# Kernel optimization log

Hardware: AMD Instinct MI355X
Metric: run time of the kernel (lower is better)

Reference implementation:

```python
import jax, jax.numpy as jnp
import numpy as np

B, S, D = 4, 4096, 256


def setup_inputs() -> dict:
    key = jax.random.key(0)
    k1, k2, k3 = jax.random.split(key, 3)
    x = jax.random.normal(k1, (B, S, D), dtype=jnp.float32)
    w_int = jax.random.randint(k2, (D, D), 0, 127, dtype=jnp.int32)  # quantized weight (out, in)
    scale = jax.random.uniform(k3, (D,), dtype=jnp.float32)          # per-output-channel scale
    return {"x": x, "w_int": w_int, "scale": scale}


def reference(x, w_int, scale):
    # self-attention: q = k = v = x, single head over feature dim D
    inv_sqrt_d = 1.0 / jnp.sqrt(jnp.asarray(D, dtype=x.dtype))
    scores = jnp.einsum('bqd,bkd->bqk', x, x) * inv_sqrt_d   # [B,S,S]
    probs = jax.nn.softmax(scores, axis=-1)
    attn = jnp.einsum('bqk,bkd->bqd', probs, x)              # [B,S,D]
    # quantized linear: dequantize then matmul (y = attn @ W^T)
    W = w_int.astype(x.dtype) * scale[:, None]               # [D_out, D_in]
    return jnp.einsum('bsd,od->bso', attn, W)
```

## Files before the change

kernel.cpp:

```cpp
#include <hip/hip_runtime.h>

typedef __bf16 bf16x8 __attribute__((ext_vector_type(8)));
typedef float f32x16 __attribute__((ext_vector_type(16)));
typedef unsigned short u16x8 __attribute__((ext_vector_type(8)));

constexpr int B = 4, S = 4096, D = 256;
constexpr float CSC = 0.09016844005556021f;

static __device__ __forceinline__ unsigned short f2bf(float f) {
  unsigned int u = __builtin_bit_cast(unsigned int, f);
  u = (u + 0x7fffu + ((u >> 16) & 1u)) >> 16;
  return (unsigned short)u;
}

static __device__ __forceinline__ float bf2f(unsigned short u) {
  unsigned int v = ((unsigned int)u) << 16;
  return __builtin_bit_cast(float, v);
}

static __device__ __forceinline__ unsigned int pk2bf(float lo, float hi) {
  unsigned int r;
  asm("v_cvt_pk_bf16_f32 %0, %1, %2" : "=v"(r) : "v"(lo), "v"(hi));
  return r;
}

static __device__ __forceinline__ void gld16(const void* g, void* l) {
  __builtin_amdgcn_global_load_lds(
      (const __attribute__((address_space(1))) unsigned int*)g,
      (__attribute__((address_space(3))) unsigned int*)l, 16, 0, 0);
}

#define FENCE_ALL()                                               \
  do {                                                            \
    asm volatile("s_waitcnt vmcnt(0) lgkmcnt(0)" ::: "memory");   \
    __builtin_amdgcn_s_barrier();                                 \
    asm volatile("" ::: "memory");                                \
  } while (0)

__global__ __launch_bounds__(256) void k_prep(const float* __restrict__ x,
                                              unsigned short* __restrict__ xbf,
                                              unsigned short* __restrict__ xK,
                                              unsigned short* __restrict__ xV) {
  __shared__ unsigned short T[64][72];
  __shared__ unsigned short R[64][72];
  int bid = blockIdx.x;
  int b = bid >> 8, rem = bid & 255;
  int s0 = (rem >> 2) * 64, d0 = (rem & 3) * 64;
  int j = threadIdx.x & 63, i0 = threadIdx.x >> 6;
#pragma unroll
  for (int k = 0; k < 16; ++k) {
    int i = k * 4 + i0;
    int idx = (b * S + s0 + i) * D + d0 + j;
    unsigned short v = f2bf(x[idx]);
    xbf[idx] = v;
    T[j][i] = v;
    R[i][j] = v;
  }
  __syncthreads();
  int t = s0 >> 6;
#pragma unroll
  for (int p = 0; p < 2; ++p) {
    int cc = p * 256 + threadIdx.x;
    int i = cc >> 3;
    int sl = (cc >> 1) & 3;
    int half = cc & 1;
    u16x8 v = *(const u16x8*)&R[i][sl * 16 + half * 8];
    int s = (d0 >> 4) + sl;
    *(u16x8*)((char*)xK + (size_t)((b * 64 + t) * 16 + s) * 2048 + i * 32 + half * 16) = v;
  }
#pragma unroll
  for (int p = 0; p < 2; ++p) {
    int cc = p * 256 + threadIdx.x;
    int dl = cc >> 3;
    int p8 = cc & 7;
    u16x8 v = *(const u16x8*)&T[dl][p8 * 8];
    int c = p8 >> 1;
    *(u16x8*)((char*)xV + (size_t)((b * 64 + t) * 4 + c) * 8192 + (d0 + dl) * 32 +
              (p8 & 1) * 16) = v;
  }
}

__global__ __launch_bounds__(256) void k_deqw(const int* __restrict__ w,
                                              unsigned short* __restrict__ wK) {
  int o = blockIdx.x, d = threadIdx.x;
  unsigned short v = f2bf((float)w[o * 256 + d]);
  wK[(d >> 4) * 4096 + o * 16 + (d & 15)] = v;
}

__global__ __launch_bounds__(512, 2) void k_attn(const unsigned short* __restrict__ xbf,
                                                 const unsigned short* __restrict__ xK,
                                                 const unsigned short* __restrict__ xV,
                                                 unsigned short* __restrict__ PO0,
                                                 unsigned short* __restrict__ PO1,
                                                 float* __restrict__ ML) {
  __shared__ __align__(16) char smem[132096];

  int tid = threadIdx.x;
  int w = tid >> 6, lane = tid & 63;
  int q5 = lane & 31, hi = lane >> 5;
  int pair = w >> 1, dh = w & 1;

  int bid = blockIdx.x;
  int swz = (bid & 7) * 32 + (bid >> 3);
  int h = swz & 1;
  int qg = swz >> 1;
  int q0 = qg * 128;
  int bat = q0 >> 12;
  int qloc = q0 & (S - 1);

  const unsigned short* Xb = xbf + (size_t)bat * (S * D);
  int qw = qloc + pair * 32;
  int koff = q5 * 32 + hi * 16;

  bf16x8 qf[16];
#pragma unroll
  for (int s = 0; s < 16; ++s)
    qf[s] = *(const bf16x8*)(Xb + (qw + q5) * D + s * 16 + hi * 8);

  f32x16 acc[8];
#pragma unroll
  for (int dt = 0; dt < 8; ++dt)
#pragma unroll
    for (int j = 0; j < 16; ++j) acc[dt][j] = 0.f;
  float l_lane = 0.f;

  const char* xKb = (const char*)xK + (size_t)(bat * 64 + h * 32) * 32768;
  const char* xVb = (const char*)xV + (size_t)(bat * 64 + h * 32) * 32768;

  auto STAGE = [&](int itile, int bb) {
    char* Kd = smem + bb * 32768;
    char* Vd = smem + 65536 + bb * 32768;
    const char* srcK = xKb + (size_t)itile * 32768;
    const char* srcV = xVb + (size_t)itile * 32768;
#pragma unroll
    for (int i = 0; i < 4; ++i) {
      int off = (w * 2 + (i >> 1)) * 2048 + (i & 1) * 1024;
      gld16(srcK + off + lane * 16, Kd + off);
    }
#pragma unroll
    for (int i = 0; i < 4; ++i) {
      int off = (w >> 1) * 8192 + ((w & 1) * 4 + i) * 1024;
      gld16(srcV + off + lane * 16, Vd + off);
    }
  };

  STAGE(0, 0);
  FENCE_ALL();

  for (int it = 0; it < 32; ++it) {
    int bb = it & 1;
    if (it + 1 < 32) STAGE(it + 1, bb ^ 1);

    const char* Kt = smem + bb * 32768 + dh * 1024 + koff;
    f32x16 sa, sb;
#pragma unroll
    for (int j = 0; j < 16; ++j) { sa[j] = 0.f; sb[j] = 0.f; }
    __builtin_amdgcn_s_setprio(1);
#pragma unroll
    for (int s = 0; s < 16; s += 2) {
      bf16x8 kfa = *(const bf16x8*)(Kt + s * 2048);
      bf16x8 kfb = *(const bf16x8*)(Kt + (s + 1) * 2048);
      sa = __builtin_amdgcn_mfma_f32_32x32x16_bf16(kfa, qf[s], sa, 0, 0, 0);
      sb = __builtin_amdgcn_mfma_f32_32x32x16_bf16(kfb, qf[s + 1], sb, 0, 0, 0);
    }
    __builtin_amdgcn_s_setprio(0);
    f32x16 st = sa + sb;

    unsigned int pk[8];
    float ps = 0.f;
#pragma unroll
    for (int a = 0; a < 8; ++a) {
      float lo = exp2f(st[2 * a] * CSC);
      float hh = exp2f(st[2 * a + 1] * CSC);
      ps += lo + hh;
      pk[a] = pk2bf(lo, hh);
    }
    l_lane += ps;

    unsigned int a0 = pk[0], b0 = pk[2];
    unsigned int a1 = pk[1], b1 = pk[3];
    unsigned int a2 = pk[4], b2 = pk[6];
    unsigned int a3 = pk[5], b3 = pk[7];
    asm volatile("v_permlane32_swap_b32 %0, %1" : "+v"(a0), "+v"(b0));
    asm volatile("v_permlane32_swap_b32 %0, %1" : "+v"(a1), "+v"(b1));
    asm volatile("v_permlane32_swap_b32 %0, %1" : "+v"(a2), "+v"(b2));
    asm volatile("v_permlane32_swap_b32 %0, %1" : "+v"(a3), "+v"(b3));
    union PA { unsigned int u[4]; bf16x8 v; };
    PA pa0, pa1;
    pa0.u[0] = a0; pa0.u[1] = a1; pa0.u[2] = b0; pa0.u[3] = b1;
    pa1.u[0] = a2; pa1.u[1] = a3; pa1.u[2] = b2; pa1.u[3] = b3;

    __builtin_amdgcn_s_setprio(1);
#pragma unroll
    for (int s2i = 0; s2i < 2; ++s2i) {
      const char* Vt = smem + 65536 + bb * 32768 + (dh * 2 + s2i) * 8192 + koff;
      bf16x8 pa = (s2i == 0) ? pa0.v : pa1.v;
#pragma unroll
      for (int dt = 0; dt < 8; ++dt) {
        bf16x8 vf = *(const bf16x8*)(Vt + dt * 1024);
        acc[dt] = __builtin_amdgcn_mfma_f32_32x32x16_bf16(vf, pa, acc[dt], 0, 0, 0);
      }
    }
    __builtin_amdgcn_s_setprio(0);

    FENCE_ALL();
  }

  float lw = l_lane + __shfl_xor(l_lane, 32, 64);
  float* LX = (float*)(smem + 131072);
  if (lane < 32) LX[w * 32 + q5] = lw;
  __syncthreads();
  float l_tot = lw + LX[(w ^ 1) * 32 + q5];
  if (dh == 0 && lane < 32) {
    int row = q0 + pair * 32 + q5;
    ML[((size_t)h * 16384 + row) * 2 + 0] = 0.f;
    ML[((size_t)h * 16384 + row) * 2 + 1] = l_tot;
  }
  __syncthreads();

  unsigned short* Pb2 = (h == 0) ? PO0 : PO1;
#pragma unroll
  for (int rh = 0; rh < 2; ++rh) {
    float* slot = (float*)(smem + w * 16384);
#pragma unroll
    for (int dt4 = 0; dt4 < 4; ++dt4) {
#pragma unroll
      for (int r = 0; r < 16; ++r) {
        int dloc = dt4 * 32 + (r & 3) + 8 * (r >> 2) + 4 * hi;
        slot[dloc * 32 + q5] = acc[rh * 4 + dt4][r];
      }
    }
    __syncthreads();
    if (dh == rh) {
      const float* pslot = (const float*)(smem + (w ^ 1) * 16384);
#pragma unroll
      for (int dt4 = 0; dt4 < 4; ++dt4) {
#pragma unroll
        for (int r = 0; r < 16; ++r) {
          int dloc = dt4 * 32 + (r & 3) + 8 * (r >> 2) + 4 * hi;
          acc[rh * 4 + dt4][r] += pslot[dloc * 32 + q5];
        }
      }
      char* E = smem + w * 16384;
#pragma unroll
      for (int dt4 = 0; dt4 < 4; ++dt4) {
#pragma unroll
        for (int a = 0; a < 4; ++a) {
          int dl = dt4 * 32 + 8 * a + 4 * hi;
          *(unsigned int*)(E + q5 * 272 + dl * 2) =
              pk2bf(acc[rh * 4 + dt4][4 * a + 0], acc[rh * 4 + dt4][4 * a + 1]);
          *(unsigned int*)(E + q5 * 272 + dl * 2 + 4) =
              pk2bf(acc[rh * 4 + dt4][4 * a + 2], acc[rh * 4 + dt4][4 * a + 3]);
        }
      }
      asm volatile("s_waitcnt lgkmcnt(0)" ::: "memory");
#pragma unroll
      for (int i = 0; i < 8; ++i) {
        int qr = i * 4 + (lane >> 4);
        int ch = lane & 15;
        u16x8 v = *(const u16x8*)(E + qr * 272 + ch * 16);
        *(u16x8*)(Pb2 + (size_t)(q0 + pair * 32 + qr) * 256 + rh * 128 + ch * 8) = v;
      }
    }
    __syncthreads();
  }
}

__global__ __launch_bounds__(512, 2) void k_gemm(const unsigned short* __restrict__ PO0,
                                                 const unsigned short* __restrict__ PO1,
                                                 const float* __restrict__ ML,
                                                 const unsigned short* __restrict__ wK,
                                                 const float* __restrict__ scale,
                                                 float* __restrict__ out) {
  __shared__ __align__(16) char Wl[131072];
  int tid = threadIdx.x;
  int w = tid >> 6, lane = tid & 63;
  int q5 = lane & 31, hi = lane >> 5;
  int msub = w & 1, oq = w >> 1;
  int m0 = blockIdx.x * 64;

#pragma unroll
  for (int i = 0; i < 16; ++i) {
    int off = (i * 512 + tid) * 16;
    gld16((const char*)wK + off, Wl + off);
  }

  int row = m0 + msub * 32 + q5;
  float il = 1.f / (ML[(size_t)row * 2 + 1] + ML[((size_t)16384 + row) * 2 + 1]);

  bf16x8 af[16];
#pragma unroll
  for (int s = 0; s < 16; ++s) {
    u16x8 a0 = *(const u16x8*)(PO0 + (size_t)row * 256 + s * 16 + hi * 8);
    u16x8 a1 = *(const u16x8*)(PO1 + (size_t)row * 256 + s * 16 + hi * 8);
    union { unsigned int u[4]; bf16x8 v; } cv;
#pragma unroll
    for (int e = 0; e < 4; ++e) {
      float lo = (bf2f(a0[2 * e]) + bf2f(a1[2 * e])) * il;
      float hh = (bf2f(a0[2 * e + 1]) + bf2f(a1[2 * e + 1])) * il;
      cv.u[e] = pk2bf(lo, hh);
    }
    af[s] = cv.v;
  }

  asm volatile("s_waitcnt vmcnt(0)" ::: "memory");
  __builtin_amdgcn_s_barrier();

  f32x16 acc[2];
#pragma unroll
  for (int t = 0; t < 2; ++t)
#pragma unroll
    for (int j = 0; j < 16; ++j) acc[t][j] = 0.f;

#pragma unroll
  for (int t = 0; t < 2; ++t) {
    int obase = (oq * 2 + t) * 32;
#pragma unroll
    for (int s = 0; s < 16; ++s) {
      bf16x8 wf = *(const bf16x8*)(Wl + s * 8192 + (obase + q5) * 32 + hi * 16);
      acc[t] = __builtin_amdgcn_mfma_f32_32x32x16_bf16(af[s], wf, acc[t], 0, 0, 0);
    }
  }

#pragma unroll
  for (int t = 0; t < 2; ++t) {
    int o = (oq * 2 + t) * 32 + q5;
    float sc = scale[o];
#pragma unroll
    for (int r = 0; r < 16; ++r) {
      int mr = m0 + msub * 32 + (r & 3) + 8 * (r >> 2) + 4 * hi;
      out[(size_t)mr * 256 + o] = acc[t][r] * sc;
    }
  }
}

extern "C" void kernel_launch(void* const* d_in, const int* in_sizes, int n_in,
                              void* d_out, int out_size, void* d_ws, size_t ws_size,
                              hipStream_t stream) {
  (void)in_sizes; (void)n_in; (void)out_size; (void)ws_size;
  const float* x = (const float*)d_in[0];
  const int* w_int = (const int*)d_in[1];
  const float* scale = (const float*)d_in[2];
  float* out = (float*)d_out;

  char* ws = (char*)d_ws;
  unsigned short* xbf = (unsigned short*)(ws);
  unsigned short* xK  = (unsigned short*)(ws + 8388608);
  unsigned short* xV  = (unsigned short*)(ws + 16777216);
  unsigned short* wK  = (unsigned short*)(ws + 25165824);
  float*          ML  = (float*)(ws + 25296896);
  unsigned short* PO0 = (unsigned short*)(ws + 25821184);
  unsigned short* PO1 = (unsigned short*)(ws + 34209792);

  k_prep<<<dim3(1024), dim3(256), 0, stream>>>(x, xbf, xK, xV);
  k_deqw<<<dim3(256), dim3(256), 0, stream>>>(w_int, wK);
  k_attn<<<dim3(256), dim3(512), 0, stream>>>(xbf, xK, xV, PO0, PO1, ML);
  k_gemm<<<dim3(256), dim3(512), 0, stream>>>(PO0, PO1, ML, wK, scale, out);
}
```

Baseline: 106.4 us.

## Split K/V/W staging layout into half-k planes to avoid LDS bank conflicts

```diff
diff --git a/kernel.cpp b/kernel.cpp
--- a/kernel.cpp
+++ b/kernel.cpp
@@ -61,22 +61,20 @@
 #pragma unroll
   for (int p = 0; p < 2; ++p) {
     int cc = p * 256 + threadIdx.x;
-    int i = cc >> 3;
-    int sl = (cc >> 1) & 3;
-    int half = cc & 1;
-    u16x8 v = *(const u16x8*)&R[i][sl * 16 + half * 8];
-    int s = (d0 >> 4) + sl;
-    *(u16x8*)((char*)xK + (size_t)((b * 64 + t) * 16 + s) * 2048 + i * 32 + half * 16) = v;
+    int sl8 = cc >> 6, row = cc & 63;
+    u16x8 v = *(const u16x8*)&R[row][sl8 * 8];
+    int dg = d0 + sl8 * 8;
+    int s = dg >> 4, hi = (dg >> 3) & 1;
+    size_t off = ((((size_t)(b * 64 + t) * 16 + s) * 2 + hi) * 64 + row) * 8;
+    *(u16x8*)(xK + off) = v;
   }
 #pragma unroll
   for (int p = 0; p < 2; ++p) {
     int cc = p * 256 + threadIdx.x;
-    int dl = cc >> 3;
-    int p8 = cc & 7;
-    u16x8 v = *(const u16x8*)&T[dl][p8 * 8];
-    int c = p8 >> 1;
-    *(u16x8*)((char*)xV + (size_t)((b * 64 + t) * 4 + c) * 8192 + (d0 + dl) * 32 +
-              (p8 & 1) * 16) = v;
+    int c = cc >> 7, hi = (cc >> 6) & 1, dl = cc & 63;
+    u16x8 v = *(const u16x8*)&T[dl][c * 16 + hi * 8];
+    size_t off = ((((size_t)(b * 64 + t) * 4 + c) * 2 + hi) * 256 + (d0 + dl)) * 8;
+    *(u16x8*)(xV + off) = v;
   }
 }
 
@@ -84,7 +82,7 @@
                                               unsigned short* __restrict__ wK) {
   int o = blockIdx.x, d = threadIdx.x;
   unsigned short v = f2bf((float)w[o * 256 + d]);
-  wK[(d >> 4) * 4096 + o * 16 + (d & 15)] = v;
+  wK[(((d >> 4) * 2 + ((d >> 3) & 1)) * 256 + o) * 8 + (d & 7)] = v;
 }
 
 __global__ __launch_bounds__(512, 2) void k_attn(const unsigned short* __restrict__ xbf,
@@ -110,7 +108,6 @@
 
   const unsigned short* Xb = xbf + (size_t)bat * (S * D);
   int qw = qloc + pair * 32;
-  int koff = q5 * 32 + hi * 16;
 
   bf16x8 qf[16];
 #pragma unroll
@@ -151,20 +148,17 @@
     int bb = it & 1;
     if (it + 1 < 32) STAGE(it + 1, bb ^ 1);
 
-    const char* Kt = smem + bb * 32768 + dh * 1024 + koff;
-    f32x16 sa, sb;
-#pragma unroll
-    for (int j = 0; j < 16; ++j) { sa[j] = 0.f; sb[j] = 0.f; }
+    const char* Kt = smem + bb * 32768 + hi * 1024 + dh * 512 + q5 * 16;
+    f32x16 st;
+#pragma unroll
+    for (int j = 0; j < 16; ++j) st[j] = 0.f;
     __builtin_amdgcn_s_setprio(1);
 #pragma unroll
-    for (int s = 0; s < 16; s += 2) {
-      bf16x8 kfa = *(const bf16x8*)(Kt + s * 2048);
-      bf16x8 kfb = *(const bf16x8*)(Kt + (s + 1) * 2048);
-      sa = __builtin_amdgcn_mfma_f32_32x32x16_bf16(kfa, qf[s], sa, 0, 0, 0);
-      sb = __builtin_amdgcn_mfma_f32_32x32x16_bf16(kfb, qf[s + 1], sb, 0, 0, 0);
+    for (int s = 0; s < 16; ++s) {
+      bf16x8 kf = *(const bf16x8*)(Kt + s * 2048);
+      st = __builtin_amdgcn_mfma_f32_32x32x16_bf16(kf, qf[s], st, 0, 0, 0);
     }
     __builtin_amdgcn_s_setprio(0);
-    f32x16 st = sa + sb;
 
     unsigned int pk[8];
     float ps = 0.f;
@@ -193,11 +187,12 @@
     __builtin_amdgcn_s_setprio(1);
 #pragma unroll
     for (int s2i = 0; s2i < 2; ++s2i) {
-      const char* Vt = smem + 65536 + bb * 32768 + (dh * 2 + s2i) * 8192 + koff;
+      const char* Vt = smem + 65536 + bb * 32768 + (dh * 2 + s2i) * 8192 +
+                       hi * 4096 + q5 * 16;
       bf16x8 pa = (s2i == 0) ? pa0.v : pa1.v;
 #pragma unroll
       for (int dt = 0; dt < 8; ++dt) {
-        bf16x8 vf = *(const bf16x8*)(Vt + dt * 1024);
+        bf16x8 vf = *(const bf16x8*)(Vt + dt * 512);
         acc[dt] = __builtin_amdgcn_mfma_f32_32x32x16_bf16(vf, pa, acc[dt], 0, 0, 0);
       }
     }
@@ -315,9 +310,10 @@
 #pragma unroll
   for (int t = 0; t < 2; ++t) {
     int obase = (oq * 2 + t) * 32;
+    const char* Wt = Wl + hi * 4096 + (obase + q5) * 16;
 #pragma unroll
     for (int s = 0; s < 16; ++s) {
-      bf16x8 wf = *(const bf16x8*)(Wl + s * 8192 + (obase + q5) * 32 + hi * 16);
+      bf16x8 wf = *(const bf16x8*)(Wt + s * 8192);
       acc[t] = __builtin_amdgcn_mfma_f32_32x32x16_bf16(af[s], wf, acc[t], 0, 0, 0);
     }
   }
```

New measurement: 104.3 us. 2.0% less time.
